# Optimization experiments

Hardware: AMD Instinct MI355X
Metric: run time of the kernel (lower is better)

Reference implementation:

```python
import jax, jax.numpy as jnp
import numpy as np

N, E, G = 20000, 100000, 64          # nodes, edges, graphs in batch
IN, HID = 63, 128                    # in_feat, hidden_feat (per-head dim)
HEADS = (8, 8, 8)                    # num_heads per GATv2 layer
NCLS = 18
EPS = 1e-5


def setup_inputs() -> dict:
    key = jax.random.key(0)
    ks = list(jax.random.split(key, 48))
    it = iter(ks)
    nrm = lambda shape, s=0.05: jax.random.normal(next(it), shape, jnp.float32) * s

    inp = {
        "h": jax.random.normal(next(it), (N, IN), jnp.float32),
        "src": jax.random.randint(next(it), (E,), 0, N, dtype=jnp.int32),
        "dst": jax.random.randint(next(it), (E,), 0, N, dtype=jnp.int32),
        "gid": jnp.sort(jax.random.randint(next(it), (N,), 0, G, dtype=jnp.int32)),
    }
    dims = [(IN, HEADS[0] * HID), (HEADS[0] * HID, HEADS[1] * HID), (HEADS[1] * HID, HEADS[2] * HID)]
    for l, (din, dout) in enumerate(dims, 1):
        H = HEADS[l - 1]
        inp[f"w_src{l}"] = nrm((din, dout))
        inp[f"b_src{l}"] = jnp.zeros((dout,), jnp.float32)
        inp[f"w_dst{l}"] = nrm((din, dout))
        inp[f"b_dst{l}"] = jnp.zeros((dout,), jnp.float32)
        inp[f"attn{l}"] = nrm((H, HID))
        inp[f"bias{l}"] = jnp.zeros((dout,), jnp.float32)
        inp[f"gamma{l}"] = jnp.ones((dout,), jnp.float32)
        inp[f"beta{l}"] = jnp.zeros((dout,), jnp.float32)
    inp["fc1_w"] = nrm((HEADS[2] * HID, HID * 8))   # 1024 -> 1024 (hidden_feat*num_heads -> hidden_feat? see note)
    inp["fc1_b"] = jnp.zeros((HID * 8,), jnp.float32)
    inp["fc2_w"] = nrm((HID * 8, 1024))
    inp["fc2_b"] = jnp.zeros((1024,), jnp.float32)
    inp["fc3_w"] = nrm((1024, NCLS))
    inp["fc3_b"] = jnp.zeros((NCLS,), jnp.float32)
    return inp


def _gatv2(h, w_src, b_src, w_dst, b_dst, attn, bias, src, dst):
    """DGL GATv2Conv forward (dropouts are identity in eval mode)."""
    H, D = attn.shape
    fs = (h @ w_src + b_src).reshape(N, H, D)   # [N,H,D]
    fd = (h @ w_dst + b_dst).reshape(N, H, D)
    e = jax.nn.leaky_relu(fs[src] + fd[dst], 0.2)          # [E,H,D], GATv2 negative_slope=0.2
    sc = jnp.einsum('ehd,hd->eh', e, attn)                 # [E,H] attention logits
    m = jax.ops.segment_max(sc, dst, num_segments=N)       # segment-softmax over in-edges
    m = jnp.where(jnp.isfinite(m), m, 0.0)                 # guard isolated nodes
    ex = jnp.exp(sc - m[dst])
    den = jax.ops.segment_sum(ex, dst, num_segments=N)
    alpha = ex / den[dst]                                  # [E,H]
    out = jax.ops.segment_sum(alpha[..., None] * fs[src], dst, num_segments=N)  # [N,H,D]
    return out.reshape(N, H * D) + bias


def _bn(x, gamma, beta):
    mu = x.mean(0)
    var = x.var(0)  # biased, as torch BN uses for normalization
    return (x - mu) * jax.lax.rsqrt(var + EPS) * gamma + beta


def _lrelu(x):
    return jax.nn.leaky_relu(x, 0.01)  # torch F.leaky_relu default slope


def reference(h, src, dst, gid,
              w_src1, b_src1, w_dst1, b_dst1, attn1, bias1, gamma1, beta1,
              w_src2, b_src2, w_dst2, b_dst2, attn2, bias2, gamma2, beta2,
              w_src3, b_src3, w_dst3, b_dst3, attn3, bias3, gamma3, beta3,
              fc1_w, fc1_b, fc2_w, fc2_b, fc3_w, fc3_b):
    x = _lrelu(_bn(_gatv2(h, w_src1, b_src1, w_dst1, b_dst1, attn1, bias1, src, dst), gamma1, beta1))
    x = _lrelu(_bn(_gatv2(x, w_src2, b_src2, w_dst2, b_dst2, attn2, bias2, src, dst), gamma2, beta2))
    x = _lrelu(_bn(_gatv2(x, w_src3, b_src3, w_dst3, b_dst3, attn3, bias3, src, dst), gamma3, beta3))
    # AvgPooling: mean over nodes of each graph
    cnt = jax.ops.segment_sum(jnp.ones((N,), x.dtype), gid, num_segments=G)
    hg = jax.ops.segment_sum(x, gid, num_segments=G) / jnp.maximum(cnt, 1.0)[:, None]  # [G, 1024]
    z = _lrelu(hg @ fc1_w + fc1_b)
    z = _lrelu(z @ fc2_w + fc2_b)
    return z @ fc3_w + fc3_b  # [G, 18]
```

## Files before the change

### kernel.cpp

```cpp
#include <hip/hip_runtime.h>
#include <math.h>

#define N_NODES 20000
#define N_PAD   20096
#define N_EDGES 100000
#define N_GRAPHS 64
#define IN_F 63
#define NHEAD 8
#define F 1024
#define NCLS 18
#define BN_EPS 1e-5f
#define BN_CHUNKS 256

typedef __attribute__((ext_vector_type(8))) _Float16 half8v;
typedef __attribute__((ext_vector_type(4))) _Float16 half4v;
typedef __attribute__((ext_vector_type(4))) float f32x4;

__global__ void k_zero_i32(int* __restrict__ p, int n) {
    int i = blockIdx.x * blockDim.x + threadIdx.x;
    if (i < n) p[i] = 0;
}

__global__ void k_count(const int* __restrict__ dst, int* __restrict__ cnt) {
    int i = blockIdx.x * blockDim.x + threadIdx.x;
    if (i < N_EDGES) atomicAdd(&cnt[dst[i]], 1);
}

__global__ void k_scan(const int* __restrict__ cnt, int* __restrict__ off,
                       const int* __restrict__ gid, int* __restrict__ gstart) {
    __shared__ int tsum[256];
    const int CH = (N_NODES + 255) / 256;
    int t = threadIdx.x;
    int s = 0;
    for (int i = 0; i < CH; ++i) {
        int idx = t * CH + i;
        if (idx < N_NODES) s += cnt[idx];
    }
    tsum[t] = s;
    __syncthreads();
    if (t == 0) {
        int acc = 0;
        for (int i = 0; i < 256; ++i) { int v = tsum[i]; tsum[i] = acc; acc += v; }
    }
    __syncthreads();
    int run = tsum[t];
    for (int i = 0; i < CH; ++i) {
        int idx = t * CH + i;
        if (idx < N_NODES) { off[idx] = run; run += cnt[idx]; }
    }
    if (t == 255) off[N_NODES] = run;
    if (t <= N_GRAPHS) {
        int lo = 0, hi = N_NODES;
        while (lo < hi) {
            int mid = (lo + hi) >> 1;
            if (gid[mid] < t) lo = mid + 1; else hi = mid;
        }
        gstart[t] = lo;
    }
}

__global__ void k_fill(const int* __restrict__ dst, const int* __restrict__ off,
                       int* __restrict__ fcnt, int* __restrict__ csr_e) {
    int i = blockIdx.x * blockDim.x + threadIdx.x;
    if (i < N_EDGES) {
        int d = dst[i];
        int p = atomicAdd(&fcnt[d], 1);
        csr_e[off[d] + p] = i;
    }
}

__global__ void k_sort_buckets(const int* __restrict__ off, int* __restrict__ csr_e) {
    int n = blockIdx.x * blockDim.x + threadIdx.x;
    if (n >= N_NODES) return;
    int b = off[n], e = off[n + 1];
    for (int i = b + 1; i < e; ++i) {
        int v = csr_e[i];
        int j = i - 1;
        while (j >= b && csr_e[j] > v) { csr_e[j + 1] = csr_e[j]; --j; }
        csr_e[j + 1] = v;
    }
}

__global__ void k_cvt_h(const float* __restrict__ h, _Float16* __restrict__ xh) {
    int idx = blockIdx.x * 256 + threadIdx.x;
    if (idx >= N_PAD * 64) return;
    int m = idx >> 6, k = idx & 63;
    float v = (m < N_NODES && k < IN_F) ? h[m * IN_F + k] : 0.f;
    xh[idx] = (_Float16)v;
}

__global__ void k_zero_pad(_Float16* __restrict__ xh) {
    int idx = blockIdx.x * 256 + threadIdx.x;
    const int total = (N_PAD - N_NODES) * F;
    if (idx < total) xh[(size_t)N_NODES * F + idx] = (_Float16)0.f;
}

__global__ void k_cvt_w2(const float* __restrict__ W0, _Float16* __restrict__ o0,
                         const float* __restrict__ W1, _Float16* __restrict__ o1,
                         int K, int Kpad) {
    const float* W = blockIdx.z ? W1 : W0;
    _Float16* wh = blockIdx.z ? o1 : o0;
    __shared__ float t[32][33];
    int kt = blockIdx.x * 32, nt = blockIdx.y * 32;
    int tx = threadIdx.x & 31, ty = threadIdx.x >> 5;
#pragma unroll
    for (int j = 0; j < 4; ++j) {
        int k = kt + ty + j * 8;
        t[ty + j * 8][tx] = (k < K) ? W[(size_t)k * F + nt + tx] : 0.f;
    }
    __syncthreads();
#pragma unroll
    for (int j = 0; j < 4; ++j) {
        int n = nt + ty + j * 8;
        wh[(size_t)n * Kpad + kt + tx] = (_Float16)t[tx][ty + j * 8];
    }
}

__global__ void k_cvt_w6(const float* __restrict__ a0, _Float16* __restrict__ b0,
                         const float* __restrict__ a1, _Float16* __restrict__ b1,
                         const float* __restrict__ a2, _Float16* __restrict__ b2,
                         const float* __restrict__ a3, _Float16* __restrict__ b3,
                         const float* __restrict__ a4, _Float16* __restrict__ b4,
                         const float* __restrict__ a5, _Float16* __restrict__ b5) {
    const float* W; _Float16* wh;
    switch (blockIdx.z) {
        case 0: W = a0; wh = b0; break;
        case 1: W = a1; wh = b1; break;
        case 2: W = a2; wh = b2; break;
        case 3: W = a3; wh = b3; break;
        case 4: W = a4; wh = b4; break;
        default: W = a5; wh = b5; break;
    }
    __shared__ float t[32][33];
    int kt = blockIdx.x * 32, nt = blockIdx.y * 32;
    int tx = threadIdx.x & 31, ty = threadIdx.x >> 5;
#pragma unroll
    for (int j = 0; j < 4; ++j) {
        int k = kt + ty + j * 8;
        t[ty + j * 8][tx] = W[(size_t)k * F + nt + tx];
    }
    __syncthreads();
#pragma unroll
    for (int j = 0; j < 4; ++j) {
        int n = nt + ty + j * 8;
        wh[(size_t)n * F + kt + tx] = (_Float16)t[tx][ty + j * 8];
    }
}

#define AS1C(p) ((const __attribute__((address_space(1))) void*)(p))
#define AS3(p)  ((__attribute__((address_space(3))) void*)(p))

__launch_bounds__(256, 2)
__global__ void k_gemm_dual(const _Float16* __restrict__ A,
                            const _Float16* __restrict__ Bs, const _Float16* __restrict__ Bd,
                            const float* __restrict__ bias_s, const float* __restrict__ bias_d,
                            _Float16* __restrict__ Cs, _Float16* __restrict__ Cd, int Kpad) {
    __shared__ _Float16 lds[24576];
    const int tid = threadIdx.x;
    const int l = tid & 63, w = tid >> 6;

    const int orig = blockIdx.y * 8 + blockIdx.x;
    const int wg = (orig & 7) * (N_PAD / 128) + (orig >> 3);
    const int by = wg >> 3, bx = wg & 7;

    const int grow = w * 32 + (l >> 3);
    const int gcol = ((l & 7) ^ (l >> 3)) << 3;
    const size_t rstep = (size_t)8 * Kpad;
    const _Float16* gA = A + (size_t)(by * 128 + grow) * Kpad + gcol;
    const _Float16* gBs = Bs + (size_t)(bx * 128 + grow) * Kpad + gcol;
    const _Float16* gBd = Bd + (size_t)(bx * 128 + grow) * Kpad + gcol;
    char* sA = (char*)lds + w * 4096;
    char* sBs = (char*)lds + 16384 + w * 4096;
    char* sBd = (char*)lds + 32768 + w * 4096;

    const int wr = (w >> 1) * 64, wc = (w & 1) * 64;
    const int frow = l & 15;
    const int swz = (l & 7) << 4;
    const int kbase = (l >> 4) * 16;

    f32x4 accS[4][4], accD[4][4];
    const f32x4 fzero = {0.f, 0.f, 0.f, 0.f};
#pragma unroll
    for (int i = 0; i < 4; ++i)
#pragma unroll
        for (int j = 0; j < 4; ++j) { accS[i][j] = fzero; accD[i][j] = fzero; }

    for (int k0 = 0; k0 < Kpad; k0 += 64) {
#pragma unroll
        for (int j = 0; j < 4; ++j) {
            __builtin_amdgcn_global_load_lds(AS1C(gA + j * rstep), AS3(sA + j * 1024), 16, 0, 0);
            __builtin_amdgcn_global_load_lds(AS1C(gBs + j * rstep), AS3(sBs + j * 1024), 16, 0, 0);
            __builtin_amdgcn_global_load_lds(AS1C(gBd + j * rstep), AS3(sBd + j * 1024), 16, 0, 0);
        }
        gA += 64; gBs += 64; gBd += 64;
        __syncthreads();

#pragma unroll
        for (int kk = 0; kk < 2; ++kk) {
            const int kb = (kk * 64 + kbase) ^ swz;
            half8v a[4];
#pragma unroll
            for (int mi = 0; mi < 4; ++mi) {
                int row = wr + mi * 16 + frow;
                a[mi] = *(const half8v*)((const char*)lds + row * 128 + kb);
            }
#pragma unroll
            for (int ni = 0; ni < 4; ++ni) {
                int rowb = wc + ni * 16 + frow;
                half8v bs = *(const half8v*)((const char*)lds + 16384 + rowb * 128 + kb);
                half8v bd = *(const half8v*)((const char*)lds + 32768 + rowb * 128 + kb);
#pragma unroll
                for (int mi = 0; mi < 4; ++mi) {
                    accS[mi][ni] = __builtin_amdgcn_mfma_f32_16x16x32_f16(a[mi], bs, accS[mi][ni], 0, 0, 0);
                    accD[mi][ni] = __builtin_amdgcn_mfma_f32_16x16x32_f16(a[mi], bd, accD[mi][ni], 0, 0, 0);
                }
            }
        }
        __syncthreads();
    }

    const int crow0 = by * 128 + wr + (l >> 4) * 4;
    const int ccol = bx * 128 + wc + (l & 15);
    float bS[4], bD[4];
#pragma unroll
    for (int ni = 0; ni < 4; ++ni) { bS[ni] = bias_s[ccol + ni * 16]; bD[ni] = bias_d[ccol + ni * 16]; }
#pragma unroll
    for (int mi = 0; mi < 4; ++mi) {
#pragma unroll
        for (int r = 0; r < 4; ++r) {
            int row = crow0 + mi * 16 + r;
            if (row < N_NODES) {
#pragma unroll
                for (int ni = 0; ni < 4; ++ni) {
                    int col = ccol + ni * 16;
                    Cs[(size_t)row * F + col] = (_Float16)(accS[mi][ni][r] + bS[ni]);
                    Cd[(size_t)row * F + col] = (_Float16)(accD[mi][ni][r] + bD[ni]);
                }
            }
        }
    }
}

__launch_bounds__(128)
__global__ void k_gat(const _Float16* __restrict__ fs, const _Float16* __restrict__ fd,
                      const int* __restrict__ off, const int* __restrict__ csr_e,
                      const int* __restrict__ src, const float* __restrict__ attn,
                      const float* __restrict__ bias, _Float16* __restrict__ y16) {
    __shared__ int s_src[128];
    const int n = blockIdx.x;
    const int t = threadIdx.x;
    const int b = off[n], e = off[n + 1];

    half8v fdv8 = *(const half8v*)(fd + (size_t)n * F + t * 8);
    float fdv[8], av[8];
    const float4 a0 = *(const float4*)(attn + (t >> 4) * 128 + (t & 15) * 8);
    const float4 a1 = *(const float4*)(attn + (t >> 4) * 128 + (t & 15) * 8 + 4);
    av[0] = a0.x; av[1] = a0.y; av[2] = a0.z; av[3] = a0.w;
    av[4] = a1.x; av[5] = a1.y; av[6] = a1.z; av[7] = a1.w;
#pragma unroll
    for (int j = 0; j < 8; ++j) fdv[j] = (float)fdv8[j];

    float m = -1e30f, den = 0.f;
    float acc[8] = {0.f, 0.f, 0.f, 0.f, 0.f, 0.f, 0.f, 0.f};

    for (int c0 = b; c0 < e; c0 += 128) {
        int ncur = e - c0; if (ncur > 128) ncur = 128;
        __syncthreads();
        if (t < ncur) s_src[t] = src[csr_e[c0 + t]];
        __syncthreads();
        half8v nxt = *(const half8v*)(fs + (size_t)s_src[0] * F + t * 8);
        for (int i = 0; i < ncur; ++i) {
            half8v cur = nxt;
            if (i + 1 < ncur)
                nxt = *(const half8v*)(fs + (size_t)s_src[i + 1] * F + t * 8);
            float f[8];
            float p = 0.f;
#pragma unroll
            for (int j = 0; j < 8; ++j) {
                f[j] = (float)cur[j];
                float v = f[j] + fdv[j];
                v = v > 0.f ? v : 0.2f * v;
                p += v * av[j];
            }
            p += __shfl_xor(p, 1);
            p += __shfl_xor(p, 2);
            p += __shfl_xor(p, 4);
            p += __shfl_xor(p, 8);
            float mn = fmaxf(m, p);
            float so = __expf(m - mn);
            float wexp = __expf(p - mn);
            den = den * so + wexp;
#pragma unroll
            for (int j = 0; j < 8; ++j) acc[j] = acc[j] * so + wexp * f[j];
            m = mn;
        }
    }
    float inv = (e > b) ? 1.f / den : 0.f;
    const float4 b0 = *(const float4*)(bias + t * 8);
    const float4 b1 = *(const float4*)(bias + t * 8 + 4);
    float bb[8] = {b0.x, b0.y, b0.z, b0.w, b1.x, b1.y, b1.z, b1.w};
    half8v o;
#pragma unroll
    for (int j = 0; j < 8; ++j) o[j] = (_Float16)(acc[j] * inv + bb[j]);
    *(half8v*)(y16 + (size_t)n * F + t * 8) = o;
}

__global__ void k_bnpart(const _Float16* __restrict__ y16, float* __restrict__ part) {
    const int ROWS = (N_NODES + BN_CHUNKS - 1) / BN_CHUNKS;
    int blk = blockIdx.x;
    int t = threadIdx.x;
    int r0 = blk * ROWS;
    int r1 = r0 + ROWS; if (r1 > N_NODES) r1 = N_NODES;
    float sx = 0.f, sy = 0.f, sz = 0.f, sw = 0.f;
    float qx = 0.f, qy = 0.f, qz = 0.f, qw = 0.f;
    for (int r = r0; r < r1; ++r) {
        half4v v = *(const half4v*)(y16 + (size_t)r * F + t * 4);
        float vx = (float)v.x, vy = (float)v.y, vz = (float)v.z, vw = (float)v.w;
        sx += vx; sy += vy; sz += vz; sw += vw;
        qx += vx * vx; qy += vy * vy; qz += vz * vz; qw += vw * vw;
    }
    float4 s4; s4.x = sx; s4.y = sy; s4.z = sz; s4.w = sw;
    float4 q4; q4.x = qx; q4.y = qy; q4.z = qz; q4.w = qw;
    *(float4*)(part + (size_t)blk * (2 * F) + t * 4) = s4;
    *(float4*)(part + (size_t)blk * (2 * F) + F + t * 4) = q4;
}

__global__ void k_bnfin(const float* __restrict__ part, const float* __restrict__ gamma,
                        const float* __restrict__ beta, float* __restrict__ scale,
                        float* __restrict__ shift) {
    int c = blockIdx.x * blockDim.x + threadIdx.x;
    if (c >= F) return;
    float s = 0.f, q = 0.f;
    for (int b = 0; b < BN_CHUNKS; ++b) {
        s += part[(size_t)b * (2 * F) + c];
        q += part[(size_t)b * (2 * F) + F + c];
    }
    float mu = s / (float)N_NODES;
    float var = q / (float)N_NODES - mu * mu;
    float sc = gamma[c] * rsqrtf(var + BN_EPS);
    scale[c] = sc;
    shift[c] = beta[c] - mu * sc;
}

__global__ void k_bnapply(const _Float16* __restrict__ y16, const float* __restrict__ scale,
                          const float* __restrict__ shift, _Float16* __restrict__ xh) {
    int i = blockIdx.x * blockDim.x + threadIdx.x;
    if (i >= N_NODES * (F / 4)) return;
    int c4 = (i & (F / 4 - 1)) * 4;
    half4v v = ((const half4v*)y16)[i];
    float4 o;
    o.x = (float)v.x * scale[c4 + 0] + shift[c4 + 0];
    o.y = (float)v.y * scale[c4 + 1] + shift[c4 + 1];
    o.z = (float)v.z * scale[c4 + 2] + shift[c4 + 2];
    o.w = (float)v.w * scale[c4 + 3] + shift[c4 + 3];
    o.x = o.x > 0.f ? o.x : 0.01f * o.x;
    o.y = o.y > 0.f ? o.y : 0.01f * o.y;
    o.z = o.z > 0.f ? o.z : 0.01f * o.z;
    o.w = o.w > 0.f ? o.w : 0.01f * o.w;
    half4v h4;
    h4.x = (_Float16)o.x; h4.y = (_Float16)o.y;
    h4.z = (_Float16)o.z; h4.w = (_Float16)o.w;
    *(half4v*)&xh[(size_t)i * 4] = h4;
}

__global__ void k_pool_bn(const _Float16* __restrict__ y16, const float* __restrict__ scale,
                          const float* __restrict__ shift, const int* __restrict__ gstart,
                          _Float16* __restrict__ hg16) {
    int g = blockIdx.y;
    int col = blockIdx.x * 256 + threadIdx.x;
    float sc = scale[col], sh = shift[col];
    int r0 = gstart[g], r1 = gstart[g + 1];
    float s = 0.f;
    for (int r = r0; r < r1; ++r) {
        float v = (float)y16[(size_t)r * F + col] * sc + sh;
        s += v > 0.f ? v : 0.01f * v;
    }
    float inv = (r1 > r0) ? 1.f / (float)(r1 - r0) : 0.f;
    hg16[(size_t)g * F + col] = (_Float16)(s * inv);
}

__launch_bounds__(256)
__global__ void k_mlp_mfma(const _Float16* __restrict__ A16, const _Float16* __restrict__ Bt,
                           const float* __restrict__ bias, _Float16* __restrict__ out16,
                           float* __restrict__ out32, int mode) {
    const int l = threadIdx.x & 63, w = threadIdx.x >> 6;
    const int bx = blockIdx.x;
    const int fko = (l >> 4) * 8;

    const _Float16* pa = A16 + (size_t)(w * 16 + (l & 15)) * 1024 + fko;
    const _Float16* pb = Bt + (size_t)(bx * 64 + (l & 15)) * 1024 + fko;

    f32x4 acc[4];
    const f32x4 fzero = {0.f, 0.f, 0.f, 0.f};
#pragma unroll
    for (int ni = 0; ni < 4; ++ni) acc[ni] = fzero;

#pragma unroll 4
    for (int k0 = 0; k0 < 1024; k0 += 32) {
        half8v a = *(const half8v*)(pa + k0);
#pragma unroll
        for (int ni = 0; ni < 4; ++ni) {
            half8v b = *(const half8v*)(pb + (size_t)ni * 16 * 1024 + k0);
            acc[ni] = __builtin_amdgcn_mfma_f32_16x16x32_f16(a, b, acc[ni], 0, 0, 0);
        }
    }

    const int row0 = w * 16 + (l >> 4) * 4;
    const int col0 = bx * 64 + (l & 15);
#pragma unroll
    for (int ni = 0; ni < 4; ++ni) {
        int col = col0 + ni * 16;
        float bb = bias[col];
#pragma unroll
        for (int r = 0; r < 4; ++r) {
            float v = acc[ni][r] + bb;
            v = v > 0.f ? v : 0.01f * v;
            if (mode == 0) out16[(size_t)(row0 + r) * 1024 + col] = (_Float16)v;
            else out32[(size_t)(row0 + r) * 1024 + col] = v;
        }
    }
}

__global__ void k_fc3(const float* __restrict__ z2, const float* __restrict__ W,
                      const float* __restrict__ b, float* __restrict__ out) {
    int gw = (blockIdx.x * blockDim.x + threadIdx.x) >> 6;
    int lane = threadIdx.x & 63;
    if (gw >= N_GRAPHS * NCLS) return;
    int row = gw / NCLS, col = gw - row * NCLS;
    float s = 0.f;
    for (int k = lane; k < 1024; k += 64) s += z2[(size_t)row * 1024 + k] * W[(size_t)k * NCLS + col];
#pragma unroll
    for (int o = 32; o; o >>= 1) s += __shfl_down(s, o);
    if (lane == 0) out[(size_t)row * NCLS + col] = s + b[col];
}

extern "C" void kernel_launch(void* const* d_in, const int* in_sizes, int n_in,
                              void* d_out, int out_size, void* d_ws, size_t ws_size,
                              hipStream_t stream) {
    const float* h = (const float*)d_in[0];
    const int* src = (const int*)d_in[1];
    const int* dst = (const int*)d_in[2];
    const int* gid = (const int*)d_in[3];

    const float *w_src[3], *b_src[3], *w_dst[3], *b_dst[3], *attn[3], *bias[3], *gamma[3], *beta[3];
    for (int l = 0; l < 3; ++l) {
        int base = 4 + l * 8;
        w_src[l] = (const float*)d_in[base + 0];
        b_src[l] = (const float*)d_in[base + 1];
        w_dst[l] = (const float*)d_in[base + 2];
        b_dst[l] = (const float*)d_in[base + 3];
        attn[l]  = (const float*)d_in[base + 4];
        bias[l]  = (const float*)d_in[base + 5];
        gamma[l] = (const float*)d_in[base + 6];
        beta[l]  = (const float*)d_in[base + 7];
    }
    const float* fc1_w = (const float*)d_in[28];
    const float* fc1_b = (const float*)d_in[29];
    const float* fc2_w = (const float*)d_in[30];
    const float* fc2_b = (const float*)d_in[31];
    const float* fc3_w = (const float*)d_in[32];
    const float* fc3_b = (const float*)d_in[33];

    char* base = (char*)d_ws;
    size_t o = 0;
    auto carve = [&](size_t bytes) -> char* {
        char* p = base + o;
        o += (bytes + 255) & ~(size_t)255;
        return p;
    };
    _Float16* fs16 = (_Float16*)carve((size_t)N_NODES * F * 2);
    _Float16* fd16 = (_Float16*)carve((size_t)N_NODES * F * 2);
    _Float16* y16 = (_Float16*)carve((size_t)N_NODES * F * 2);
    _Float16* xh = (_Float16*)carve((size_t)N_PAD * F * 2);
    _Float16* w1s = (_Float16*)carve((size_t)F * 64 * 2);
    _Float16* w1d = (_Float16*)carve((size_t)F * 64 * 2);
    _Float16* w2s = (_Float16*)carve((size_t)F * F * 2);
    _Float16* w2d = (_Float16*)carve((size_t)F * F * 2);
    _Float16* w3s = (_Float16*)carve((size_t)F * F * 2);
    _Float16* w3d = (_Float16*)carve((size_t)F * F * 2);
    _Float16* fc1h = (_Float16*)carve((size_t)F * F * 2);
    _Float16* fc2h = (_Float16*)carve((size_t)F * F * 2);
    int* cnt = (int*)carve((size_t)2 * N_NODES * 4);
    int* fcnt = cnt + N_NODES;
    int* off = (int*)carve((size_t)(N_NODES + 1) * 4);
    int* csr_e = (int*)carve((size_t)N_EDGES * 4);
    float* part = (float*)carve((size_t)BN_CHUNKS * 2 * F * 4);
    float* scale = (float*)carve(F * 4);
    float* shift = (float*)carve(F * 4);
    int* gstart = (int*)carve((N_GRAPHS + 1) * 4);
    _Float16* hg16 = (_Float16*)carve((size_t)N_GRAPHS * F * 2);
    _Float16* z1h = (_Float16*)carve((size_t)N_GRAPHS * F * 2);
    float* z2 = (float*)carve((size_t)N_GRAPHS * F * 4);
    (void)ws_size;

    k_zero_i32<<<(2 * N_NODES + 255) / 256, 256, 0, stream>>>(cnt, 2 * N_NODES);
    k_count<<<(N_EDGES + 255) / 256, 256, 0, stream>>>(dst, cnt);
    k_scan<<<1, 256, 0, stream>>>(cnt, off, gid, gstart);
    k_fill<<<(N_EDGES + 255) / 256, 256, 0, stream>>>(dst, off, fcnt, csr_e);
    k_sort_buckets<<<(N_NODES + 255) / 256, 256, 0, stream>>>(off, csr_e);

    k_cvt_h<<<(N_PAD * 64 + 255) / 256, 256, 0, stream>>>(h, xh);
    k_zero_pad<<<((N_PAD - N_NODES) * F + 255) / 256, 256, 0, stream>>>(xh);
    k_cvt_w2<<<dim3(2, F / 32, 2), 256, 0, stream>>>(w_src[0], w1s, w_dst[0], w1d, IN_F, 64);
    k_cvt_w6<<<dim3(F / 32, F / 32, 6), 256, 0, stream>>>(
        w_src[1], w2s, w_dst[1], w2d, w_src[2], w3s, w_dst[2], w3d, fc1_w, fc1h, fc2_w, fc2h);

    const dim3 ggrid(8, N_PAD / 128);
    const _Float16* ws16[3] = {w1s, w2s, w3s};
    const _Float16* wd16[3] = {w1d, w2d, w3d};
    for (int l = 0; l < 3; ++l) {
        const int Kp = (l == 0) ? 64 : F;
        k_gemm_dual<<<ggrid, 256, 0, stream>>>(xh, ws16[l], wd16[l], b_src[l], b_dst[l],
                                               fs16, fd16, Kp);
        k_gat<<<N_NODES, 128, 0, stream>>>(fs16, fd16, off, csr_e, src, attn[l], bias[l], y16);
        k_bnpart<<<BN_CHUNKS, 256, 0, stream>>>(y16, part);
        k_bnfin<<<F / 256, 256, 0, stream>>>(part, gamma[l], beta[l], scale, shift);
        if (l < 2)
            k_bnapply<<<(N_NODES * (F / 4) + 255) / 256, 256, 0, stream>>>(y16, scale, shift, xh);
    }

    k_pool_bn<<<dim3(4, N_GRAPHS), 256, 0, stream>>>(y16, scale, shift, gstart, hg16);
    k_mlp_mfma<<<16, 256, 0, stream>>>(hg16, fc1h, fc1_b, z1h, nullptr, 0);
    k_mlp_mfma<<<16, 256, 0, stream>>>(z1h, fc2h, fc2_b, nullptr, z2, 1);
    k_fc3<<<(N_GRAPHS * NCLS * 64 + 255) / 256, 256, 0, stream>>>(z2, fc3_w, fc3_b, (float*)d_out);
}
```

Baseline: 754.4 us.

## Merge prep kernels, widen BN loads to 8 halves, enlarge scan block

Several small changes land together. The zero kernel becomes hipMemsetAsync, and the h conversion and pad zeroing are merged into one launch. The scan now uses 1024 threads. BN partial sums and BN apply read 8 halves per load instead of 4, and bnpart splits rows between two half-blocks, which doubles the partial buffer read by bnfin. The aim is fewer launches and wider memory accesses in the bandwidth-bound BN passes, at the cost of a longer serial prefix loop in the scan and twice as many partials to reduce.

```diff
diff --git a/kernel.cpp b/kernel.cpp
--- a/kernel.cpp
+++ b/kernel.cpp
@@ -16,11 +16,6 @@
 typedef __attribute__((ext_vector_type(4))) _Float16 half4v;
 typedef __attribute__((ext_vector_type(4))) float f32x4;
 
-__global__ void k_zero_i32(int* __restrict__ p, int n) {
-    int i = blockIdx.x * blockDim.x + threadIdx.x;
-    if (i < n) p[i] = 0;
-}
-
 __global__ void k_count(const int* __restrict__ dst, int* __restrict__ cnt) {
     int i = blockIdx.x * blockDim.x + threadIdx.x;
     if (i < N_EDGES) atomicAdd(&cnt[dst[i]], 1);
@@ -28,8 +23,8 @@
 
 __global__ void k_scan(const int* __restrict__ cnt, int* __restrict__ off,
                        const int* __restrict__ gid, int* __restrict__ gstart) {
-    __shared__ int tsum[256];
-    const int CH = (N_NODES + 255) / 256;
+    __shared__ int tsum[1024];
+    const int CH = (N_NODES + 1023) / 1024;
     int t = threadIdx.x;
     int s = 0;
     for (int i = 0; i < CH; ++i) {
@@ -40,7 +35,7 @@
     __syncthreads();
     if (t == 0) {
         int acc = 0;
-        for (int i = 0; i < 256; ++i) { int v = tsum[i]; tsum[i] = acc; acc += v; }
+        for (int i = 0; i < 1024; ++i) { int v = tsum[i]; tsum[i] = acc; acc += v; }
     }
     __syncthreads();
     int run = tsum[t];
@@ -48,7 +43,7 @@
         int idx = t * CH + i;
         if (idx < N_NODES) { off[idx] = run; run += cnt[idx]; }
     }
-    if (t == 255) off[N_NODES] = run;
+    if (t == 1023) off[N_NODES] = run;
     if (t <= N_GRAPHS) {
         int lo = 0, hi = N_NODES;
         while (lo < hi) {
@@ -81,18 +76,17 @@
     }
 }
 
-__global__ void k_cvt_h(const float* __restrict__ h, _Float16* __restrict__ xh) {
+__global__ void k_prep(const float* __restrict__ h, _Float16* __restrict__ xh) {
+    const int T1 = N_PAD * 64;
+    const int T2 = (N_PAD - N_NODES) * F;
     int idx = blockIdx.x * 256 + threadIdx.x;
-    if (idx >= N_PAD * 64) return;
-    int m = idx >> 6, k = idx & 63;
-    float v = (m < N_NODES && k < IN_F) ? h[m * IN_F + k] : 0.f;
-    xh[idx] = (_Float16)v;
-}
-
-__global__ void k_zero_pad(_Float16* __restrict__ xh) {
-    int idx = blockIdx.x * 256 + threadIdx.x;
-    const int total = (N_PAD - N_NODES) * F;
-    if (idx < total) xh[(size_t)N_NODES * F + idx] = (_Float16)0.f;
+    if (idx < T1) {
+        int m = idx >> 6, k = idx & 63;
+        float v = (m < N_NODES && k < IN_F) ? h[m * IN_F + k] : 0.f;
+        xh[idx] = (_Float16)v;
+    } else if (idx < T1 + T2) {
+        xh[(size_t)N_NODES * F + (idx - T1)] = (_Float16)0.f;
+    }
 }
 
 __global__ void k_cvt_w2(const float* __restrict__ W0, _Float16* __restrict__ o0,
@@ -309,20 +303,25 @@
     const int ROWS = (N_NODES + BN_CHUNKS - 1) / BN_CHUNKS;
     int blk = blockIdx.x;
     int t = threadIdx.x;
-    int r0 = blk * ROWS;
-    int r1 = r0 + ROWS; if (r1 > N_NODES) r1 = N_NODES;
-    float sx = 0.f, sy = 0.f, sz = 0.f, sw = 0.f;
-    float qx = 0.f, qy = 0.f, qz = 0.f, qw = 0.f;
-    for (int r = r0; r < r1; ++r) {
-        half4v v = *(const half4v*)(y16 + (size_t)r * F + t * 4);
-        float vx = (float)v.x, vy = (float)v.y, vz = (float)v.z, vw = (float)v.w;
-        sx += vx; sy += vy; sz += vz; sw += vw;
-        qx += vx * vx; qy += vy * vy; qz += vz * vz; qw += vw * vw;
-    }
-    float4 s4; s4.x = sx; s4.y = sy; s4.z = sz; s4.w = sw;
-    float4 q4; q4.x = qx; q4.y = qy; q4.z = qz; q4.w = qw;
-    *(float4*)(part + (size_t)blk * (2 * F) + t * 4) = s4;
-    *(float4*)(part + (size_t)blk * (2 * F) + F + t * 4) = q4;
+    int sub = t >> 7;
+    int c8 = (t & 127) * 8;
+    int r0 = blk * ROWS + sub;
+    int r1 = blk * ROWS + ROWS; if (r1 > N_NODES) r1 = N_NODES;
+    float s[8] = {}, q[8] = {};
+    for (int r = r0; r < r1; r += 2) {
+        half8v v = *(const half8v*)(y16 + (size_t)r * F + c8);
+#pragma unroll
+        for (int j = 0; j < 8; ++j) {
+            float f = (float)v[j];
+            s[j] += f; q[j] += f * f;
+        }
+    }
+    float* ps = part + (size_t)(blk * 2 + sub) * (2 * F);
+#pragma unroll
+    for (int j = 0; j < 8; ++j) {
+        ps[c8 + j] = s[j];
+        ps[F + c8 + j] = q[j];
+    }
 }
 
 __global__ void k_bnfin(const float* __restrict__ part, const float* __restrict__ gamma,
@@ -331,7 +330,7 @@
     int c = blockIdx.x * blockDim.x + threadIdx.x;
     if (c >= F) return;
     float s = 0.f, q = 0.f;
-    for (int b = 0; b < BN_CHUNKS; ++b) {
+    for (int b = 0; b < BN_CHUNKS * 2; ++b) {
         s += part[(size_t)b * (2 * F) + c];
         q += part[(size_t)b * (2 * F) + F + c];
     }
@@ -345,22 +344,17 @@
 __global__ void k_bnapply(const _Float16* __restrict__ y16, const float* __restrict__ scale,
                           const float* __restrict__ shift, _Float16* __restrict__ xh) {
     int i = blockIdx.x * blockDim.x + threadIdx.x;
-    if (i >= N_NODES * (F / 4)) return;
-    int c4 = (i & (F / 4 - 1)) * 4;
-    half4v v = ((const half4v*)y16)[i];
-    float4 o;
-    o.x = (float)v.x * scale[c4 + 0] + shift[c4 + 0];
-    o.y = (float)v.y * scale[c4 + 1] + shift[c4 + 1];
-    o.z = (float)v.z * scale[c4 + 2] + shift[c4 + 2];
-    o.w = (float)v.w * scale[c4 + 3] + shift[c4 + 3];
-    o.x = o.x > 0.f ? o.x : 0.01f * o.x;
-    o.y = o.y > 0.f ? o.y : 0.01f * o.y;
-    o.z = o.z > 0.f ? o.z : 0.01f * o.z;
-    o.w = o.w > 0.f ? o.w : 0.01f * o.w;
-    half4v h4;
-    h4.x = (_Float16)o.x; h4.y = (_Float16)o.y;
-    h4.z = (_Float16)o.z; h4.w = (_Float16)o.w;
-    *(half4v*)&xh[(size_t)i * 4] = h4;
+    if (i >= N_NODES * (F / 8)) return;
+    int c8 = (i & (F / 8 - 1)) * 8;
+    half8v v = ((const half8v*)y16)[i];
+    half8v h8;
+#pragma unroll
+    for (int j = 0; j < 8; ++j) {
+        float o = (float)v[j] * scale[c8 + j] + shift[c8 + j];
+        o = o > 0.f ? o : 0.01f * o;
+        h8[j] = (_Float16)o;
+    }
+    ((half8v*)xh)[i] = h8;
 }
 
 __global__ void k_pool_bn(const _Float16* __restrict__ y16, const float* __restrict__ scale,
@@ -484,7 +478,7 @@
     int* fcnt = cnt + N_NODES;
     int* off = (int*)carve((size_t)(N_NODES + 1) * 4);
     int* csr_e = (int*)carve((size_t)N_EDGES * 4);
-    float* part = (float*)carve((size_t)BN_CHUNKS * 2 * F * 4);
+    float* part = (float*)carve((size_t)BN_CHUNKS * 2 * 2 * F * 4);
     float* scale = (float*)carve(F * 4);
     float* shift = (float*)carve(F * 4);
     int* gstart = (int*)carve((N_GRAPHS + 1) * 4);
@@ -493,14 +487,14 @@
     float* z2 = (float*)carve((size_t)N_GRAPHS * F * 4);
     (void)ws_size;
 
-    k_zero_i32<<<(2 * N_NODES + 255) / 256, 256, 0, stream>>>(cnt, 2 * N_NODES);
+    hipMemsetAsync(cnt, 0, (size_t)2 * N_NODES * 4, stream);
     k_count<<<(N_EDGES + 255) / 256, 256, 0, stream>>>(dst, cnt);
-    k_scan<<<1, 256, 0, stream>>>(cnt, off, gid, gstart);
+    k_scan<<<1, 1024, 0, stream>>>(cnt, off, gid, gstart);
     k_fill<<<(N_EDGES + 255) / 256, 256, 0, stream>>>(dst, off, fcnt, csr_e);
     k_sort_buckets<<<(N_NODES + 255) / 256, 256, 0, stream>>>(off, csr_e);
 
-    k_cvt_h<<<(N_PAD * 64 + 255) / 256, 256, 0, stream>>>(h, xh);
-    k_zero_pad<<<((N_PAD - N_NODES) * F + 255) / 256, 256, 0, stream>>>(xh);
+    const int PREP_T = N_PAD * 64 + (N_PAD - N_NODES) * F;
+    k_prep<<<(PREP_T + 255) / 256, 256, 0, stream>>>(h, xh);
     k_cvt_w2<<<dim3(2, F / 32, 2), 256, 0, stream>>>(w_src[0], w1s, w_dst[0], w1d, IN_F, 64);
     k_cvt_w6<<<dim3(F / 32, F / 32, 6), 256, 0, stream>>>(
         w_src[1], w2s, w_dst[1], w2d, w_src[2], w3s, w_dst[2], w3d, fc1_w, fc1h, fc2_w, fc2h);
@@ -516,7 +510,7 @@
         k_bnpart<<<BN_CHUNKS, 256, 0, stream>>>(y16, part);
         k_bnfin<<<F / 256, 256, 0, stream>>>(part, gamma[l], beta[l], scale, shift);
         if (l < 2)
-            k_bnapply<<<(N_NODES * (F / 4) + 255) / 256, 256, 0, stream>>>(y16, scale, shift, xh);
+            k_bnapply<<<(N_NODES * (F / 8) + 255) / 256, 256, 0, stream>>>(y16, scale, shift, xh);
     }
 
     k_pool_bn<<<dim3(4, N_GRAPHS), 256, 0, stream>>>(y16, scale, shift, gstart, hg16);
```

Measured after the change: 770.5 us. +2.1%, slower.
